# Kernel tuning notes

Hardware: AMD Instinct MI355X
Metric: run time of the kernel (lower is better)

Reference implementation:

```python
import jax, jax.numpy as jnp
import numpy as np

D_MODEL = 1024
NUM_HEADS = 16
D_K = D_MODEL // NUM_HEADS
BATCH = 2
SEQ = 2048


def setup_inputs() -> dict:
    key = jax.random.key(0)
    ks = jax.random.split(key, 11)
    s = 1.0 / np.sqrt(D_MODEL)
    return {
        "query": jax.random.normal(ks[0], (BATCH, SEQ, D_MODEL), jnp.float32),
        "key_": jax.random.normal(ks[1], (BATCH, SEQ, D_MODEL), jnp.float32),
        "value": jax.random.normal(ks[2], (BATCH, SEQ, D_MODEL), jnp.float32),
        "w_q": jax.random.uniform(ks[3], (D_MODEL, D_MODEL), jnp.float32, -s, s),
        "b_q": jax.random.uniform(ks[4], (D_MODEL,), jnp.float32, -s, s),
        "w_k": jax.random.uniform(ks[5], (D_MODEL, D_MODEL), jnp.float32, -s, s),
        "b_k": jax.random.uniform(ks[6], (D_MODEL,), jnp.float32, -s, s),
        "w_v": jax.random.uniform(ks[7], (D_MODEL, D_MODEL), jnp.float32, -s, s),
        "b_v": jax.random.uniform(ks[8], (D_MODEL,), jnp.float32, -s, s),
        "w_o": jax.random.uniform(ks[9], (D_MODEL, D_MODEL), jnp.float32, -s, s),
        "b_o": jax.random.uniform(ks[10], (D_MODEL,), jnp.float32, -s, s),
    }


def reference(query, key_, value, w_q, b_q, w_k, b_k, w_v, b_v, w_o, b_o):
    B, S, D = query.shape
    H, dk = NUM_HEADS, D_K

    def proj(x, w, b):
        # torch Linear: x @ w.T + b ; reshape to (B, H, S, dk)
        return (x @ w.T + b).reshape(B, S, H, dk).transpose(0, 2, 1, 3)

    Q = proj(query, w_q, b_q)
    K = proj(key_, w_k, b_k)
    V = proj(value, w_v, b_v)

    scores = jnp.einsum("bhqd,bhkd->bhqk", Q, K) / jnp.sqrt(jnp.float32(dk))
    attn = jax.nn.softmax(scores, axis=-1)  # dropout is identity in eval
    ctx = jnp.einsum("bhqk,bhkd->bhqd", attn, V)
    ctx = ctx.transpose(0, 2, 1, 3).reshape(B, S, D)
    out = ctx @ w_o.T + b_o
    return out
```

## Files before the change

kernel.cpp:

```cpp
#include <hip/hip_runtime.h>
#include <cstdint>
#include <cstddef>

typedef unsigned short u16;
typedef short bf16x8 __attribute__((ext_vector_type(8)));
typedef unsigned short u16x8 __attribute__((ext_vector_type(8)));
typedef float f32x4 __attribute__((ext_vector_type(4)));

#define NHEAD 16
#define SEQ 2048
#define DMODEL 1024
#define BATCH 2
#define QSCALE 0.18033688011112042f

__device__ __forceinline__ float exp2_fast(float x) {
  return __builtin_amdgcn_exp2f(x);
}

__device__ __forceinline__ u16 f2bf(float f) {
  union { float f; unsigned u; } v; v.f = f;
  return (u16)((v.u + 0x7fffu + ((v.u >> 16) & 1u)) >> 16);
}

__device__ __forceinline__ int swz(int row, int colbyte) {
  return (row << 7) + (colbyte ^ ((row & 7) << 4));
}

__device__ __forceinline__ void load_lds16(const void* g, void* lds) {
  __builtin_amdgcn_global_load_lds(
      (const __attribute__((address_space(1))) unsigned int*)g,
      (__attribute__((address_space(3))) unsigned int*)lds, 16, 0, 0);
}

__global__ __launch_bounds__(256) void convall(
    const float* __restrict__ q, const float* __restrict__ k, const float* __restrict__ v,
    const float* __restrict__ wq, const float* __restrict__ wk,
    const float* __restrict__ wv, const float* __restrict__ wo,
    u16* __restrict__ Xq, u16* __restrict__ Xk, u16* __restrict__ Xv,
    u16* __restrict__ Wq, u16* __restrict__ Wk, u16* __restrict__ Wv,
    u16* __restrict__ Wo) {
  int bid = blockIdx.x;
  const float* in;
  u16* out;
  int local;
  if (bid < 6144) {
    int a = bid >> 11;
    local = bid & 2047;
    in = a == 0 ? q : a == 1 ? k : v;
    out = a == 0 ? Xq : a == 1 ? Xk : Xv;
  } else {
    int bb = bid - 6144;
    int a = bb >> 9;
    local = bb & 511;
    in = a == 0 ? wq : a == 1 ? wk : a == 2 ? wv : wo;
    out = a == 0 ? Wq : a == 1 ? Wk : a == 2 ? Wv : Wo;
  }
  int i = local * 256 + threadIdx.x;
  const float4* p = (const float4*)in + (size_t)i * 2;
  float4 a4 = p[0], b4 = p[1];
  u16x8 o;
  o[0] = f2bf(a4.x); o[1] = f2bf(a4.y); o[2] = f2bf(a4.z); o[3] = f2bf(a4.w);
  o[4] = f2bf(b4.x); o[5] = f2bf(b4.y); o[6] = f2bf(b4.z); o[7] = f2bf(b4.w);
  *((u16x8*)out + i) = o;
}

__global__ __launch_bounds__(256) void gemm_qkv(
    const u16* __restrict__ A0, const u16* __restrict__ A1, const u16* __restrict__ A2,
    const u16* __restrict__ W0, const u16* __restrict__ W1, const u16* __restrict__ W2,
    const float* __restrict__ b0, const float* __restrict__ b1, const float* __restrict__ b2,
    u16* __restrict__ C0, u16* __restrict__ C1, u16* __restrict__ C2) {
  constexpr int K = 1024;
  __shared__ u16 Ash[128 * 32];
  __shared__ u16 Bsh[128 * 32];
  const int z = blockIdx.z;
  const u16* A = z == 0 ? A0 : z == 1 ? A1 : A2;
  const u16* W = z == 0 ? W0 : z == 1 ? W1 : W2;
  const float* bias = z == 0 ? b0 : z == 1 ? b1 : b2;
  u16* C = z == 0 ? C0 : z == 1 ? C1 : C2;
  const float scale = z == 0 ? QSCALE : 1.0f;

  const int t = threadIdx.x;
  const int w = t >> 6;
  const int l = t & 63;
  const int m0 = blockIdx.y * 128;
  const int n0 = blockIdx.x * 128;
  const int wm = (w >> 1) * 64;
  const int wn = (w & 1) * 64;
  const int lr = l & 15;
  const int hi = l >> 4;
  const int lk = hi * 8;
  const int srow = l >> 2;
  const int scol = (l & 3) * 8;

  f32x4 acc[4][4] = {};

  for (int k0 = 0; k0 < K; k0 += 32) {
#pragma unroll
    for (int c = 0; c < 2; ++c) {
      int ra = (c * 4 + w) * 16 + srow;
      load_lds16(A + (size_t)(m0 + ra) * K + k0 + scol, &Ash[(c * 4 + w) * 512]);
      load_lds16(W + (size_t)(n0 + ra) * K + k0 + scol, &Bsh[(c * 4 + w) * 512]);
    }
    __syncthreads();
    bf16x8 af[4], bfr[4];
#pragma unroll
    for (int i = 0; i < 4; ++i)
      af[i] = *(const bf16x8*)&Ash[(wm + i * 16 + lr) * 32 + lk];
#pragma unroll
    for (int j = 0; j < 4; ++j)
      bfr[j] = *(const bf16x8*)&Bsh[(wn + j * 16 + lr) * 32 + lk];
#pragma unroll
    for (int i = 0; i < 4; ++i)
#pragma unroll
      for (int j = 0; j < 4; ++j)
        acc[i][j] = __builtin_amdgcn_mfma_f32_16x16x32_bf16(af[i], bfr[j], acc[i][j], 0, 0, 0);
    __syncthreads();
  }

#pragma unroll
  for (int i = 0; i < 4; ++i)
#pragma unroll
    for (int j = 0; j < 4; ++j)
#pragma unroll
      for (int r = 0; r < 4; ++r) {
        int row = m0 + wm + i * 16 + hi * 4 + r;
        int col = n0 + wn + j * 16 + lr;
        float v = (acc[i][j][r] + bias[col]) * scale;
        int b = row >> 11, s = row & 2047;
        int h = col >> 6, d = col & 63;
        C[(((size_t)(b * NHEAD + h) * SEQ + s) << 6) + d] = f2bf(v);
      }
}

__global__ __launch_bounds__(256) void gemm_o(const u16* __restrict__ A,
                                              const u16* __restrict__ W,
                                              const float* __restrict__ bias,
                                              float* __restrict__ C) {
  constexpr int K = 1024;
  __shared__ u16 Ash[64 * 32];
  __shared__ u16 Bsh[128 * 32];
  const int t = threadIdx.x;
  const int w = t >> 6;
  const int l = t & 63;
  const int m0 = blockIdx.y * 64;
  const int n0 = blockIdx.x * 128;
  const int wm = (w >> 1) * 32;
  const int wn = (w & 1) * 64;
  const int lr = l & 15;
  const int hi = l >> 4;
  const int lk = hi * 8;
  const int srow = l >> 2;
  const int scol = (l & 3) * 8;

  f32x4 acc[2][4] = {};

  for (int k0 = 0; k0 < K; k0 += 32) {
    {
      int ra = w * 16 + srow;
      load_lds16(A + (size_t)(m0 + ra) * K + k0 + scol, &Ash[w * 512]);
    }
#pragma unroll
    for (int c = 0; c < 2; ++c) {
      int rb = (c * 4 + w) * 16 + srow;
      load_lds16(W + (size_t)(n0 + rb) * K + k0 + scol, &Bsh[(c * 4 + w) * 512]);
    }
    __syncthreads();
    bf16x8 af[2], bfr[4];
#pragma unroll
    for (int i = 0; i < 2; ++i)
      af[i] = *(const bf16x8*)&Ash[(wm + i * 16 + lr) * 32 + lk];
#pragma unroll
    for (int j = 0; j < 4; ++j)
      bfr[j] = *(const bf16x8*)&Bsh[(wn + j * 16 + lr) * 32 + lk];
#pragma unroll
    for (int i = 0; i < 2; ++i)
#pragma unroll
      for (int j = 0; j < 4; ++j)
        acc[i][j] = __builtin_amdgcn_mfma_f32_16x16x32_bf16(af[i], bfr[j], acc[i][j], 0, 0, 0);
    __syncthreads();
  }

#pragma unroll
  for (int i = 0; i < 2; ++i)
#pragma unroll
    for (int j = 0; j < 4; ++j)
#pragma unroll
      for (int r = 0; r < 4; ++r) {
        int row = m0 + wm + i * 16 + hi * 4 + r;
        int col = n0 + wn + j * 16 + lr;
        C[(size_t)row * DMODEL + col] = acc[i][j][r] + bias[col];
      }
}

__global__ __launch_bounds__(256) void transpose_v(const u16* __restrict__ V,
                                                   u16* __restrict__ Vt) {
  __shared__ u16 tile[64][72];
  int st = blockIdx.x, bh = blockIdx.y;
  int t = threadIdx.x;
  {
    int s = t >> 2, part = (t & 3) * 16;
    const u16* g = V + (((size_t)bh * SEQ + st * 64 + s) << 6) + part;
    u16x8 v0 = *(const u16x8*)&g[0];
    u16x8 v1 = *(const u16x8*)&g[8];
    *(u16x8*)&tile[s][part] = v0;
    *(u16x8*)&tile[s][part + 8] = v1;
  }
  __syncthreads();
  {
    int d = t >> 2, sp = (t & 3) * 16;
    u16x8 o0, o1;
#pragma unroll
    for (int j = 0; j < 8; ++j) {
      int c0 = sp + j, c1 = sp + 8 + j;
      o0[j] = tile[(c0 & 3) * 16 + (c0 >> 2)][d];
      o1[j] = tile[(c1 & 3) * 16 + (c1 >> 2)][d];
    }
    u16* out = Vt + ((size_t)bh * 64 + d) * SEQ + st * 64 + sp;
    *(u16x8*)&out[0] = o0;
    *(u16x8*)&out[8] = o1;
  }
}

__device__ __forceinline__ void attn_tile(
    int kt, bool pf, const u16* Kg, const u16* Vg, int srow, int scb,
    char* QsB, char* KsC, char* VsC, char* KsN, char* VsN,
    bf16x8 (&qf)[2][2], f32x4 (&acc)[2][4], float (&lsum)[2][4],
    int w, int lr, int hi) {
  u16x8 nk0, nk1, nv0, nv1;
  if (pf) {
    const u16* kg = Kg + (kt + 1) * 4096;
    const u16* vg = Vg + (kt + 1) * 64;
    nk0 = *(const u16x8*)&kg[srow * 64 + scb / 2];
    nk1 = *(const u16x8*)&kg[srow * 64 + scb / 2 + 8];
    nv0 = *(const u16x8*)&vg[(size_t)srow * SEQ + scb / 2];
    nv1 = *(const u16x8*)&vg[(size_t)srow * SEQ + scb / 2 + 8];
  }

  f32x4 sc[2][4] = {};
  __builtin_amdgcn_s_setprio(1);
#pragma unroll
  for (int ks = 0; ks < 2; ++ks) {
    bf16x8 kb[4];
#pragma unroll
    for (int nt = 0; nt < 4; ++nt)
      kb[nt] = *(const bf16x8*)(KsC + swz(nt * 16 + lr, ks * 64 + hi * 16));
#pragma unroll
    for (int mt = 0; mt < 2; ++mt)
#pragma unroll
      for (int nt = 0; nt < 4; ++nt)
        sc[mt][nt] = __builtin_amdgcn_mfma_f32_16x16x32_bf16(qf[mt][ks], kb[nt], sc[mt][nt], 0, 0, 0);
  }
  __builtin_amdgcn_s_setprio(0);

#pragma unroll
  for (int mt = 0; mt < 2; ++mt)
#pragma unroll
    for (int r = 0; r < 4; ++r) {
      int prow = w * 32 + mt * 16 + hi * 4 + r;
      float p0 = exp2_fast(sc[mt][0][r]);
      float p1 = exp2_fast(sc[mt][1][r]);
      float p2 = exp2_fast(sc[mt][2][r]);
      float p3 = exp2_fast(sc[mt][3][r]);
      lsum[mt][r] += (p0 + p1) + (p2 + p3);
      uint2 pk;
      asm("v_cvt_pk_bf16_f32 %0, %1, %2" : "=v"(pk.x) : "v"(p0), "v"(p1));
      asm("v_cvt_pk_bf16_f32 %0, %1, %2" : "=v"(pk.y) : "v"(p2), "v"(p3));
      *(uint2*)(QsB + swz(prow, lr * 8)) = pk;
    }

  asm volatile("" ::: "memory");

  __builtin_amdgcn_s_setprio(1);
#pragma unroll
  for (int ks = 0; ks < 2; ++ks) {
    bf16x8 pa[2], vb[4];
#pragma unroll
    for (int mt = 0; mt < 2; ++mt)
      pa[mt] = *(const bf16x8*)(QsB + swz(w * 32 + mt * 16 + lr, ks * 64 + hi * 16));
#pragma unroll
    for (int nt = 0; nt < 4; ++nt)
      vb[nt] = *(const bf16x8*)(VsC + swz(nt * 16 + lr, ks * 64 + hi * 16));
#pragma unroll
    for (int mt = 0; mt < 2; ++mt)
#pragma unroll
      for (int nt = 0; nt < 4; ++nt)
        acc[mt][nt] = __builtin_amdgcn_mfma_f32_16x16x32_bf16(pa[mt], vb[nt], acc[mt][nt], 0, 0, 0);
  }
  __builtin_amdgcn_s_setprio(0);

  if (pf) {
    *(u16x8*)(KsN + swz(srow, scb)) = nk0;
    *(u16x8*)(KsN + swz(srow, scb + 16)) = nk1;
    *(u16x8*)(VsN + swz(srow, scb)) = nv0;
    *(u16x8*)(VsN + swz(srow, scb + 16)) = nv1;
  }
  __syncthreads();
}

__global__ __launch_bounds__(256) void attn(const u16* __restrict__ Q,
                                            const u16* __restrict__ K,
                                            const u16* __restrict__ Vt,
                                            u16* __restrict__ ctx) {
  __shared__ u16 Qs[128 * 64];
  __shared__ u16 Ks[2][64 * 64];
  __shared__ u16 Vs[2][64 * 64];
  char* const QsB = (char*)Qs;

  const int t = threadIdx.x, w = t >> 6, l = t & 63;
  const int lr = l & 15, hi = l >> 4;

  const int bid = blockIdx.x;
  const int idx = bid >> 3;
  const int bh = (bid & 7) * 4 + (idx >> 4);
  const int q0 = (idx & 15) * 128;

  const u16* Qg = Q + ((size_t)bh * SEQ + q0) * 64;
  const u16* Kg = K + (size_t)bh * SEQ * 64;
  const u16* Vg = Vt + (size_t)bh * 64 * SEQ;

#pragma unroll
  for (int i = 0; i < 4; ++i) {
    int c = i * 256 + t;
    int row = c >> 3, cb = (c & 7) * 16;
    u16x8 qv = *(const u16x8*)&Qg[row * 64 + cb / 2];
    *(u16x8*)(QsB + swz(row, cb)) = qv;
  }
  const int srow = t >> 2;
  const int scb = (t & 3) * 32;
  {
    u16x8 k0 = *(const u16x8*)&Kg[srow * 64 + scb / 2];
    u16x8 k1 = *(const u16x8*)&Kg[srow * 64 + scb / 2 + 8];
    u16x8 v0 = *(const u16x8*)&Vg[(size_t)srow * SEQ + scb / 2];
    u16x8 v1 = *(const u16x8*)&Vg[(size_t)srow * SEQ + scb / 2 + 8];
    char* KsB = (char*)Ks[0];
    char* VsB = (char*)Vs[0];
    *(u16x8*)(KsB + swz(srow, scb)) = k0;
    *(u16x8*)(KsB + swz(srow, scb + 16)) = k1;
    *(u16x8*)(VsB + swz(srow, scb)) = v0;
    *(u16x8*)(VsB + swz(srow, scb + 16)) = v1;
  }
  __syncthreads();

  bf16x8 qf[2][2];
#pragma unroll
  for (int mt = 0; mt < 2; ++mt)
#pragma unroll
    for (int ks = 0; ks < 2; ++ks)
      qf[mt][ks] = *(const bf16x8*)(QsB + swz(w * 32 + mt * 16 + lr, ks * 64 + hi * 16));

  f32x4 acc[2][4] = {};
  float lsum[2][4] = {{0.f, 0.f, 0.f, 0.f}, {0.f, 0.f, 0.f, 0.f}};

  for (int kt2 = 0; kt2 < SEQ / 128; ++kt2) {
    attn_tile(2 * kt2, true, Kg, Vg, srow, scb, QsB,
              (char*)Ks[0], (char*)Vs[0], (char*)Ks[1], (char*)Vs[1],
              qf, acc, lsum, w, lr, hi);
    attn_tile(2 * kt2 + 1, kt2 < SEQ / 128 - 1, Kg, Vg, srow, scb, QsB,
              (char*)Ks[1], (char*)Vs[1], (char*)Ks[0], (char*)Vs[0],
              qf, acc, lsum, w, lr, hi);
  }

  const int b = bh >> 4, h = bh & 15;
#pragma unroll
  for (int mt = 0; mt < 2; ++mt)
#pragma unroll
    for (int r = 0; r < 4; ++r) {
      float s = lsum[mt][r];
      s += __shfl_xor(s, 1);
      s += __shfl_xor(s, 2);
      s += __shfl_xor(s, 4);
      s += __shfl_xor(s, 8);
      float inv = 1.0f / s;
      int srow_ = q0 + w * 32 + mt * 16 + hi * 4 + r;
#pragma unroll
      for (int nt = 0; nt < 4; ++nt) {
        int d = nt * 16 + lr;
        ctx[((size_t)(b * SEQ + srow_)) * DMODEL + h * 64 + d] =
            f2bf(acc[mt][nt][r] * inv);
      }
    }
}

extern "C" void kernel_launch(void* const* d_in, const int* in_sizes, int n_in,
                              void* d_out, int out_size, void* d_ws, size_t ws_size,
                              hipStream_t stream) {
  const float* q  = (const float*)d_in[0];
  const float* k  = (const float*)d_in[1];
  const float* v  = (const float*)d_in[2];
  const float* wq = (const float*)d_in[3];
  const float* bq = (const float*)d_in[4];
  const float* wk = (const float*)d_in[5];
  const float* bk = (const float*)d_in[6];
  const float* wv = (const float*)d_in[7];
  const float* bv = (const float*)d_in[8];
  const float* wo = (const float*)d_in[9];
  const float* bo = (const float*)d_in[10];

  const size_t XB = (size_t)4096 * 1024 * 2;
  const size_t WB = (size_t)1024 * 1024 * 2;
  char* ws = (char*)d_ws;
  u16* Xq = (u16*)(ws);
  u16* Xk = (u16*)(ws + XB);
  u16* Xv = (u16*)(ws + 2 * XB);
  u16* Wq = (u16*)(ws + 3 * XB);
  u16* Wk = (u16*)(ws + 3 * XB + WB);
  u16* Wv = (u16*)(ws + 3 * XB + 2 * WB);
  u16* Wo = (u16*)(ws + 3 * XB + 3 * WB);
  u16* Qb = (u16*)(ws + 4 * XB);
  u16* Kb = (u16*)(ws + 5 * XB);
  u16* Vb = (u16*)(ws + 6 * XB);
  u16* Vtb = Xk;
  u16* ctxb = Xq;

  convall<<<8192, 256, 0, stream>>>(q, k, v, wq, wk, wv, wo,
                                    Xq, Xk, Xv, Wq, Wk, Wv, Wo);

  gemm_qkv<<<dim3(8, 32, 3), 256, 0, stream>>>(Xq, Xk, Xv, Wq, Wk, Wv,
                                               bq, bk, bv, Qb, Kb, Vb);

  transpose_v<<<dim3(SEQ / 64, BATCH * NHEAD), 256, 0, stream>>>(Vb, Vtb);

  attn<<<512, 256, 0, stream>>>(Qb, Kb, Vtb, ctxb);

  gemm_o<<<dim3(8, 64), 256, 0, stream>>>(ctxb, Wo, bo, (float*)d_out);
}
```

Before: 129.5 us.

## Process two KV tiles per barrier with four-stage LDS ring buffer

Grows the K/V shared-memory ring from two to four tile buffers and restructures the attention main loop so each barrier covers two 64-key tiles. Global loads for the next pair of tiles are issued before computing the current pair and stored to LDS afterwards. The goal is to halve the number of block-wide synchronisations and give memory loads more time to complete behind the MFMA work. In exchange, LDS use per block rises substantially, which may lower the number of resident blocks per CU, and more registers are held live for the prefetched tiles.

```diff
diff --git a/kernel.cpp b/kernel.cpp
--- a/kernel.cpp
+++ b/kernel.cpp
@@ -221,21 +221,32 @@
   }
 }
 
-__device__ __forceinline__ void attn_tile(
-    int kt, bool pf, const u16* Kg, const u16* Vg, int srow, int scb,
-    char* QsB, char* KsC, char* VsC, char* KsN, char* VsN,
+struct KVregs { u16x8 k0, k1, v0, v1; };
+
+__device__ __forceinline__ KVregs kv_load(const u16* Kg, const u16* Vg, int kt,
+                                          int srow, int scb) {
+  KVregs r;
+  const u16* kg = Kg + kt * 4096;
+  const u16* vg = Vg + kt * 64;
+  r.k0 = *(const u16x8*)&kg[srow * 64 + scb / 2];
+  r.k1 = *(const u16x8*)&kg[srow * 64 + scb / 2 + 8];
+  r.v0 = *(const u16x8*)&vg[(size_t)srow * SEQ + scb / 2];
+  r.v1 = *(const u16x8*)&vg[(size_t)srow * SEQ + scb / 2 + 8];
+  return r;
+}
+
+__device__ __forceinline__ void kv_store(char* KsB, char* VsB, const KVregs& r,
+                                         int srow, int scb) {
+  *(u16x8*)(KsB + swz(srow, scb)) = r.k0;
+  *(u16x8*)(KsB + swz(srow, scb + 16)) = r.k1;
+  *(u16x8*)(VsB + swz(srow, scb)) = r.v0;
+  *(u16x8*)(VsB + swz(srow, scb + 16)) = r.v1;
+}
+
+__device__ __forceinline__ void attn_tile2(
+    char* QsB, char* KsC, char* VsC,
     bf16x8 (&qf)[2][2], f32x4 (&acc)[2][4], float (&lsum)[2][4],
     int w, int lr, int hi) {
-  u16x8 nk0, nk1, nv0, nv1;
-  if (pf) {
-    const u16* kg = Kg + (kt + 1) * 4096;
-    const u16* vg = Vg + (kt + 1) * 64;
-    nk0 = *(const u16x8*)&kg[srow * 64 + scb / 2];
-    nk1 = *(const u16x8*)&kg[srow * 64 + scb / 2 + 8];
-    nv0 = *(const u16x8*)&vg[(size_t)srow * SEQ + scb / 2];
-    nv1 = *(const u16x8*)&vg[(size_t)srow * SEQ + scb / 2 + 8];
-  }
-
   f32x4 sc[2][4] = {};
   __builtin_amdgcn_s_setprio(1);
 #pragma unroll
@@ -288,13 +299,7 @@
   }
   __builtin_amdgcn_s_setprio(0);
 
-  if (pf) {
-    *(u16x8*)(KsN + swz(srow, scb)) = nk0;
-    *(u16x8*)(KsN + swz(srow, scb + 16)) = nk1;
-    *(u16x8*)(VsN + swz(srow, scb)) = nv0;
-    *(u16x8*)(VsN + swz(srow, scb + 16)) = nv1;
-  }
-  __syncthreads();
+  asm volatile("" ::: "memory");
 }
 
 __global__ __launch_bounds__(256) void attn(const u16* __restrict__ Q,
@@ -302,9 +307,17 @@
                                             const u16* __restrict__ Vt,
                                             u16* __restrict__ ctx) {
   __shared__ u16 Qs[128 * 64];
-  __shared__ u16 Ks[2][64 * 64];
-  __shared__ u16 Vs[2][64 * 64];
+  __shared__ u16 Ks[4][64 * 64];
+  __shared__ u16 Vs[4][64 * 64];
   char* const QsB = (char*)Qs;
+  char* const Ks0 = (char*)Ks[0];
+  char* const Ks1 = (char*)Ks[1];
+  char* const Ks2 = (char*)Ks[2];
+  char* const Ks3 = (char*)Ks[3];
+  char* const Vs0 = (char*)Vs[0];
+  char* const Vs1 = (char*)Vs[1];
+  char* const Vs2 = (char*)Vs[2];
+  char* const Vs3 = (char*)Vs[3];
 
   const int t = threadIdx.x, w = t >> 6, l = t & 63;
   const int lr = l & 15, hi = l >> 4;
@@ -327,18 +340,8 @@
   }
   const int srow = t >> 2;
   const int scb = (t & 3) * 32;
-  {
-    u16x8 k0 = *(const u16x8*)&Kg[srow * 64 + scb / 2];
-    u16x8 k1 = *(const u16x8*)&Kg[srow * 64 + scb / 2 + 8];
-    u16x8 v0 = *(const u16x8*)&Vg[(size_t)srow * SEQ + scb / 2];
-    u16x8 v1 = *(const u16x8*)&Vg[(size_t)srow * SEQ + scb / 2 + 8];
-    char* KsB = (char*)Ks[0];
-    char* VsB = (char*)Vs[0];
-    *(u16x8*)(KsB + swz(srow, scb)) = k0;
-    *(u16x8*)(KsB + swz(srow, scb + 16)) = k1;
-    *(u16x8*)(VsB + swz(srow, scb)) = v0;
-    *(u16x8*)(VsB + swz(srow, scb + 16)) = v1;
-  }
+  kv_store(Ks0, Vs0, kv_load(Kg, Vg, 0, srow, scb), srow, scb);
+  kv_store(Ks1, Vs1, kv_load(Kg, Vg, 1, srow, scb), srow, scb);
   __syncthreads();
 
   bf16x8 qf[2][2];
@@ -351,13 +354,28 @@
   f32x4 acc[2][4] = {};
   float lsum[2][4] = {{0.f, 0.f, 0.f, 0.f}, {0.f, 0.f, 0.f, 0.f}};
 
-  for (int kt2 = 0; kt2 < SEQ / 128; ++kt2) {
-    attn_tile(2 * kt2, true, Kg, Vg, srow, scb, QsB,
-              (char*)Ks[0], (char*)Vs[0], (char*)Ks[1], (char*)Vs[1],
-              qf, acc, lsum, w, lr, hi);
-    attn_tile(2 * kt2 + 1, kt2 < SEQ / 128 - 1, Kg, Vg, srow, scb, QsB,
-              (char*)Ks[1], (char*)Vs[1], (char*)Ks[0], (char*)Vs[0],
-              qf, acc, lsum, w, lr, hi);
+  for (int j2 = 0; j2 < 8; ++j2) {
+    const int base = j2 * 4;
+    KVregs a = kv_load(Kg, Vg, base + 2, srow, scb);
+    KVregs b = kv_load(Kg, Vg, base + 3, srow, scb);
+    attn_tile2(QsB, Ks0, Vs0, qf, acc, lsum, w, lr, hi);
+    attn_tile2(QsB, Ks1, Vs1, qf, acc, lsum, w, lr, hi);
+    kv_store(Ks2, Vs2, a, srow, scb);
+    kv_store(Ks3, Vs3, b, srow, scb);
+    __syncthreads();
+    const bool pf = (j2 < 7);
+    KVregs c, d;
+    if (pf) {
+      c = kv_load(Kg, Vg, base + 4, srow, scb);
+      d = kv_load(Kg, Vg, base + 5, srow, scb);
+    }
+    attn_tile2(QsB, Ks2, Vs2, qf, acc, lsum, w, lr, hi);
+    attn_tile2(QsB, Ks3, Vs3, qf, acc, lsum, w, lr, hi);
+    if (pf) {
+      kv_store(Ks0, Vs0, c, srow, scb);
+      kv_store(Ks1, Vs1, d, srow, scb);
+    }
+    __syncthreads();
   }
 
   const int b = bh >> 4, h = bh & 15;
```

Measured after the change: 140.6 us. 1.09x slower.

## Fuse V transpose into QKV GEMM epilogue and widen K-step with swizzled LDS

Applied to the files above, without the earlier changes.

The QKV GEMM now loads 64-wide K tiles into XOR-swizzled shared memory, halving the number of barrier-separated iterations and avoiding LDS bank conflicts. For the V projection, the epilogue stages results through shared memory and writes the permuted, transposed layout the attention kernel expects directly, so the separate transpose_v launch and its extra global round-trip go away. This doubles LDS use per block, which may reduce occupancy, and adds extra barriers to the V epilogue.

```diff
diff --git a/kernel.cpp b/kernel.cpp
--- a/kernel.cpp
+++ b/kernel.cpp
@@ -70,8 +70,9 @@
     const float* __restrict__ b0, const float* __restrict__ b1, const float* __restrict__ b2,
     u16* __restrict__ C0, u16* __restrict__ C1, u16* __restrict__ C2) {
   constexpr int K = 1024;
-  __shared__ u16 Ash[128 * 32];
-  __shared__ u16 Bsh[128 * 32];
+  __shared__ __align__(16) char pool[32768];
+  u16* const Ash = (u16*)pool;
+  u16* const Bsh = (u16*)(pool + 16384);
   const int z = blockIdx.z;
   const u16* A = z == 0 ? A0 : z == 1 ? A1 : A2;
   const u16* W = z == 0 ? W0 : z == 1 ? W1 : W2;
@@ -88,48 +89,98 @@
   const int wn = (w & 1) * 64;
   const int lr = l & 15;
   const int hi = l >> 4;
-  const int lk = hi * 8;
-  const int srow = l >> 2;
-  const int scol = (l & 3) * 8;
+  const int sr = l >> 3;
+  const int scbl = (l & 7) * 16;
 
   f32x4 acc[4][4] = {};
 
-  for (int k0 = 0; k0 < K; k0 += 32) {
-#pragma unroll
-    for (int c = 0; c < 2; ++c) {
-      int ra = (c * 4 + w) * 16 + srow;
-      load_lds16(A + (size_t)(m0 + ra) * K + k0 + scol, &Ash[(c * 4 + w) * 512]);
-      load_lds16(W + (size_t)(n0 + ra) * K + k0 + scol, &Bsh[(c * 4 + w) * 512]);
+  for (int k0 = 0; k0 < K; k0 += 64) {
+#pragma unroll
+    for (int c = 0; c < 4; ++c) {
+      int round = c * 4 + w;
+      int ra = round * 8 + sr;
+      int cbs = scbl ^ ((ra & 7) << 4);
+      load_lds16(A + (size_t)(m0 + ra) * K + k0 + cbs / 2, (char*)Ash + round * 1024);
+      load_lds16(W + (size_t)(n0 + ra) * K + k0 + cbs / 2, (char*)Bsh + round * 1024);
     }
     __syncthreads();
-    bf16x8 af[4], bfr[4];
+#pragma unroll
+    for (int s = 0; s < 2; ++s) {
+      bf16x8 af[4], bfr[4];
+#pragma unroll
+      for (int i = 0; i < 4; ++i) {
+        int row = wm + i * 16 + lr;
+        af[i] = *(const bf16x8*)((char*)Ash + row * 128 +
+                                 ((s * 64 + hi * 16) ^ ((row & 7) << 4)));
+      }
+#pragma unroll
+      for (int j = 0; j < 4; ++j) {
+        int row = wn + j * 16 + lr;
+        bfr[j] = *(const bf16x8*)((char*)Bsh + row * 128 +
+                                  ((s * 64 + hi * 16) ^ ((row & 7) << 4)));
+      }
+#pragma unroll
+      for (int i = 0; i < 4; ++i)
+#pragma unroll
+        for (int j = 0; j < 4; ++j)
+          acc[i][j] = __builtin_amdgcn_mfma_f32_16x16x32_bf16(af[i], bfr[j], acc[i][j], 0, 0, 0);
+    }
+    __syncthreads();
+  }
+
+  if (z != 2) {
 #pragma unroll
     for (int i = 0; i < 4; ++i)
-      af[i] = *(const bf16x8*)&Ash[(wm + i * 16 + lr) * 32 + lk];
-#pragma unroll
-    for (int j = 0; j < 4; ++j)
-      bfr[j] = *(const bf16x8*)&Bsh[(wn + j * 16 + lr) * 32 + lk];
-#pragma unroll
-    for (int i = 0; i < 4; ++i)
 #pragma unroll
       for (int j = 0; j < 4; ++j)
-        acc[i][j] = __builtin_amdgcn_mfma_f32_16x16x32_bf16(af[i], bfr[j], acc[i][j], 0, 0, 0);
-    __syncthreads();
-  }
-
-#pragma unroll
-  for (int i = 0; i < 4; ++i)
-#pragma unroll
-    for (int j = 0; j < 4; ++j)
-#pragma unroll
-      for (int r = 0; r < 4; ++r) {
-        int row = m0 + wm + i * 16 + hi * 4 + r;
-        int col = n0 + wn + j * 16 + lr;
-        float v = (acc[i][j][r] + bias[col]) * scale;
-        int b = row >> 11, s = row & 2047;
-        int h = col >> 6, d = col & 63;
-        C[(((size_t)(b * NHEAD + h) * SEQ + s) << 6) + d] = f2bf(v);
-      }
+#pragma unroll
+        for (int r = 0; r < 4; ++r) {
+          int row = m0 + wm + i * 16 + hi * 4 + r;
+          int col = n0 + wn + j * 16 + lr;
+          float v = (acc[i][j][r] + bias[col]) * scale;
+          int b = row >> 11, s = row & 2047;
+          int h = col >> 6, d = col & 63;
+          C[(((size_t)(b * NHEAD + h) * SEQ + s) << 6) + d] = f2bf(v);
+        }
+  } else {
+    asm volatile("" ::: "memory");
+    u16 (*Tsh)[137] = (u16 (*)[137])pool;
+    const int b = m0 >> 11, s0 = m0 & 2047;
+    const int h0 = n0 >> 6;
+#pragma unroll
+    for (int p = 0; p < 2; ++p) {
+      if ((w & 1) == p) {
+#pragma unroll
+        for (int i = 0; i < 4; ++i)
+#pragma unroll
+          for (int j = 0; j < 4; ++j)
+#pragma unroll
+            for (int r = 0; r < 4; ++r) {
+              int rl = wm + i * 16 + hi * 4 + r;
+              int dl = j * 16 + lr;
+              Tsh[dl][rl] = f2bf(acc[i][j][r] + bias[n0 + p * 64 + dl]);
+            }
+      }
+      __syncthreads();
+      {
+        int d = t >> 2, cpart = (t & 3) * 16;
+        u16* outp = C + ((size_t)(b * NHEAD + h0 + p) * 64 + d) * SEQ + s0;
+#pragma unroll
+        for (int blk = 0; blk < 2; ++blk)
+#pragma unroll
+          for (int vv = 0; vv < 2; ++vv) {
+            u16x8 o;
+#pragma unroll
+            for (int jj = 0; jj < 8; ++jj) {
+              int c = cpart + vv * 8 + jj;
+              o[jj] = Tsh[d][blk * 64 + (c & 3) * 16 + (c >> 2)];
+            }
+            *(u16x8*)&outp[blk * 64 + cpart + vv * 8] = o;
+          }
+      }
+      __syncthreads();
+    }
+  }
 }
 
 __global__ __launch_bounds__(256) void gemm_o(const u16* __restrict__ A,
@@ -192,35 +243,6 @@
       }
 }
 
-__global__ __launch_bounds__(256) void transpose_v(const u16* __restrict__ V,
-                                                   u16* __restrict__ Vt) {
-  __shared__ u16 tile[64][72];
-  int st = blockIdx.x, bh = blockIdx.y;
-  int t = threadIdx.x;
-  {
-    int s = t >> 2, part = (t & 3) * 16;
-    const u16* g = V + (((size_t)bh * SEQ + st * 64 + s) << 6) + part;
-    u16x8 v0 = *(const u16x8*)&g[0];
-    u16x8 v1 = *(const u16x8*)&g[8];
-    *(u16x8*)&tile[s][part] = v0;
-    *(u16x8*)&tile[s][part + 8] = v1;
-  }
-  __syncthreads();
-  {
-    int d = t >> 2, sp = (t & 3) * 16;
-    u16x8 o0, o1;
-#pragma unroll
-    for (int j = 0; j < 8; ++j) {
-      int c0 = sp + j, c1 = sp + 8 + j;
-      o0[j] = tile[(c0 & 3) * 16 + (c0 >> 2)][d];
-      o1[j] = tile[(c1 & 3) * 16 + (c1 >> 2)][d];
-    }
-    u16* out = Vt + ((size_t)bh * 64 + d) * SEQ + st * 64 + sp;
-    *(u16x8*)&out[0] = o0;
-    *(u16x8*)&out[8] = o1;
-  }
-}
-
 __device__ __forceinline__ void attn_tile(
     int kt, bool pf, const u16* Kg, const u16* Vg, int srow, int scb,
     char* QsB, char* KsC, char* VsC, char* KsN, char* VsN,
@@ -408,17 +430,14 @@
   u16* Wo = (u16*)(ws + 3 * XB + 3 * WB);
   u16* Qb = (u16*)(ws + 4 * XB);
   u16* Kb = (u16*)(ws + 5 * XB);
-  u16* Vb = (u16*)(ws + 6 * XB);
-  u16* Vtb = Xk;
+  u16* Vtb = (u16*)(ws + 6 * XB);
   u16* ctxb = Xq;
 
   convall<<<8192, 256, 0, stream>>>(q, k, v, wq, wk, wv, wo,
                                     Xq, Xk, Xv, Wq, Wk, Wv, Wo);
 
   gemm_qkv<<<dim3(8, 32, 3), 256, 0, stream>>>(Xq, Xk, Xv, Wq, Wk, Wv,
-                                               bq, bk, bv, Qb, Kb, Vb);
-
-  transpose_v<<<dim3(SEQ / 64, BATCH * NHEAD), 256, 0, stream>>>(Vb, Vtb);
+                                               bq, bk, bv, Qb, Kb, Vtb);
 
   attn<<<512, 256, 0, stream>>>(Qb, Kb, Vtb, ctxb);
 
```

Measured after the change: 136.0 us. 5.0% more time.
